# Kernel optimization log

Measured on AMD Instinct MI355X. Metric: run time of the kernel, lower is better.

Reference implementation:

```python
import jax, jax.numpy as jnp
import numpy as np
import math

N, D, H, E = 4096, 128, 8, 131072
HD = D // H  # head_dim = 16
SCALE = 1.0 / math.sqrt(HD)


def ln(x, g, b, eps=1e-5):
    m = x.mean(-1, keepdims=True)
    v = ((x - m) ** 2).mean(-1, keepdims=True)
    return (x - m) * jax.lax.rsqrt(v + eps) * g + b


def setup_inputs() -> dict:
    key = jax.random.key(0)
    ks = iter(jax.random.split(key, 40))

    def lin(out_d, in_d):
        w = jax.random.normal(next(ks), (out_d, in_d), jnp.float32) / math.sqrt(in_d)
        b = jnp.zeros((out_d,), jnp.float32)
        return w, b

    x = jax.random.normal(next(ks), (N, D), jnp.float32)
    edge_index = jax.random.randint(next(ks), (2, E), 0, N, dtype=jnp.int64)
    wq_l, bq_l = lin(D, D); wk_l, bk_l = lin(D, D); wv_l, bv_l = lin(D, D)
    wg, bg = lin(D, 2 * D)
    wq_g, bq_g = lin(D, D); wk_g, bk_g = lin(D, D); wv_g, bv_g = lin(D, D)
    wo_g, bo_g = lin(D, D)
    wf, bf = lin(D, 2 * D)
    gf = jnp.ones((D,), jnp.float32); betaf = jnp.zeros((D,), jnp.float32)
    w1, b1 = lin(4 * D, D); w2, b2 = lin(D, 4 * D)
    g1 = jnp.ones((D,), jnp.float32); be1 = jnp.zeros((D,), jnp.float32)
    g2 = jnp.ones((D,), jnp.float32); be2 = jnp.zeros((D,), jnp.float32)
    return dict(x=x, edge_index=edge_index,
                wq_l=wq_l, bq_l=bq_l, wk_l=wk_l, bk_l=bk_l, wv_l=wv_l, bv_l=bv_l,
                wg=wg, bg=bg,
                wq_g=wq_g, bq_g=bq_g, wk_g=wk_g, bk_g=bk_g, wv_g=wv_g, bv_g=bv_g,
                wo_g=wo_g, bo_g=bo_g,
                wf=wf, bf=bf, gf=gf, betaf=betaf,
                w1=w1, b1=b1, w2=w2, b2=b2,
                g1=g1, be1=be1, g2=g2, be2=be2)


def reference(x, edge_index, wq_l, bq_l, wk_l, bk_l, wv_l, bv_l, wg, bg,
              wq_g, bq_g, wk_g, bk_g, wv_g, bv_g, wo_g, bo_g,
              wf, bf, gf, betaf, w1, b1, w2, b2, g1, be1, g2, be2):
    src, dst = edge_index[0], edge_index[1]  # PyG: j=source, i=target
    # ---- local edge-indexed multi-head attention (GraphInteractionModule) ----
    Q = (x @ wq_l.T + bq_l).reshape(N, H, HD)
    K = (x @ wk_l.T + bk_l).reshape(N, H, HD)
    V = (x @ wv_l.T + bv_l).reshape(N, H, HD)
    attn = (Q[dst] * K[src]).sum(-1) * SCALE            # [E, H]
    m = jax.ops.segment_max(attn, dst, num_segments=N)  # [N, H]
    e = jnp.exp(attn - m[dst])
    s = jax.ops.segment_sum(e, dst, num_segments=N)
    alpha = e / s[dst]                                  # segment softmax over edges into each dst
    agg = jax.ops.segment_sum(V[src] * alpha[..., None], dst, num_segments=N).reshape(N, D)
    gate = jax.nn.sigmoid(jnp.concatenate([x, agg], axis=-1) @ wg.T + bg)
    local = gate * agg + (1.0 - gate) * x
    # ---- global dense MHA over all nodes (B=1) ----
    xn = ln(x, g1, be1)
    q = (xn @ wq_g.T + bq_g).reshape(N, H, HD)
    k = (xn @ wk_g.T + bk_g).reshape(N, H, HD)
    v = (xn @ wv_g.T + bv_g).reshape(N, H, HD)
    scores = jnp.einsum('nhd,mhd->hnm', q, k) * SCALE   # [H, N, N]
    p = jax.nn.softmax(scores, axis=-1)
    go = jnp.einsum('hnm,mhd->nhd', p, v).reshape(N, D) @ wo_g.T + bo_g
    # ---- fusion + residual + FFN ----
    fused = jax.nn.relu(ln(jnp.concatenate([local, go], axis=-1) @ wf.T + bf, gf, betaf))
    h = x + fused
    h2 = ln(h, g2, be2)
    out = h + (jax.nn.gelu(h2 @ w1.T + b1, approximate=False) @ w2.T + b2)
    return out
```

## Files before the change

kernel.cpp:

```cpp
#include <hip/hip_runtime.h>
#include <math.h>

#define NN 4096
#define DM 128
#define NE 131072
#define BCAP 96
#define QSCALE 0.36067376022224085f
#define ESCALE 0.36067376022224085f

typedef short short8 __attribute__((ext_vector_type(8)));
typedef float f32x4  __attribute__((ext_vector_type(4)));
typedef unsigned int uint4v __attribute__((ext_vector_type(4)));

static __device__ __forceinline__ unsigned pk2(float lo, float hi) {
  union { float f; unsigned u; } a, b; a.f = lo; b.f = hi;
  return __builtin_amdgcn_perm(b.u + 0x8000u, a.u + 0x8000u, 0x07060302u);
}
static __device__ __forceinline__ unsigned pkp(float lo, float hi) {
  union { float f; unsigned u; } a, b; a.f = lo; b.f = hi;
  return __builtin_amdgcn_perm(b.u, a.u, 0x07060302u);
}
static __device__ __forceinline__ unsigned short f2bh(float f) {
  union { float f; unsigned u; } v; v.f = f;
  return (unsigned short)((v.u + 0x8000u) >> 16);
}
static __device__ __forceinline__ float b2f16(unsigned short u) {
  union { unsigned u; float f; } v; v.u = ((unsigned)u) << 16; return v.f;
}
static __device__ __forceinline__ float blo(unsigned u) {
  union { unsigned u; float f; } v; v.u = u << 16; return v.f;
}
static __device__ __forceinline__ float bhi(unsigned u) {
  union { unsigned u; float f; } v; v.u = u & 0xffff0000u; return v.f;
}
static __device__ __forceinline__ short8 cvt8(float4 a, float4 b) {
  uint4v u;
  u.x = pk2(a.x, a.y); u.y = pk2(a.z, a.w);
  u.z = pk2(b.x, b.y); u.w = pk2(b.z, b.w);
  return __builtin_bit_cast(short8, u);
}
static __device__ __forceinline__ int detect64(const int* __restrict__ EI) {
  int v = EI[2 * (threadIdx.x & 63) + 1];
  for (int off = 1; off < 64; off <<= 1) v |= __shfl_xor(v, off);
  return (v == 0) ? 1 : 0;
}

__global__ __launch_bounds__(256) void k_fill(float* __restrict__ out, float v, int n) {
  int i = blockIdx.x * 256 + threadIdx.x;
  if (i < n) out[i] = v;
}

#define LN1(V, GV, BV) V = (V - mean) * rstd * GV + BV
__global__ __launch_bounds__(256) void gemm_six(
    const float* __restrict__ X,
    const float* __restrict__ G1, const float* __restrict__ Be1,
    const float* __restrict__ W0, const float* __restrict__ W1, const float* __restrict__ W2,
    const float* __restrict__ W3, const float* __restrict__ W4, const float* __restrict__ W5,
    const float* __restrict__ B0, const float* __restrict__ B1, const float* __restrict__ B2,
    const float* __restrict__ B3, const float* __restrict__ B4, const float* __restrict__ B5,
    void* __restrict__ O0, void* __restrict__ O1, void* __restrict__ O2,
    void* __restrict__ O3, void* __restrict__ O4, void* __restrict__ O5,
    int* __restrict__ deg,
    const float* __restrict__ WFp, const float* __restrict__ WOg, const float* __restrict__ BOg,
    float* __restrict__ WCp, float* __restrict__ BFp,
    const int* __restrict__ EI, int* __restrict__ EL)
{
  __shared__ short Asm[2][64][40];
  __shared__ short Wsm[2][64][40];
  if (blockIdx.y == 13) {
    int is64 = detect64(EI);
    int base = blockIdx.x * 2048 + threadIdx.x;
#pragma unroll
    for (int r = 0; r < 8; r++) {
      int e = base + r * 256;
      int d = is64 ? EI[2*(NE+e)] : EI[NE+e];
      d = min(max(d, 0), NN-1);
      int slot = atomicAdd(&deg[d], 1);
      if (slot < BCAP) EL[d * BCAP + slot] = e;
    }
    return;
  }
  if (blockIdx.y == 12) {
    if (blockIdx.x >= 16) return;
    const int c = threadIdx.x & 127;
    const int f0 = blockIdx.x * 8 + (threadIdx.x >> 7) * 4;
    const float* wf0 = WFp + (size_t)(f0 + 0) * 256 + 128;
    const float* wf1 = WFp + (size_t)(f0 + 1) * 256 + 128;
    const float* wf2 = WFp + (size_t)(f0 + 2) * 256 + 128;
    const float* wf3 = WFp + (size_t)(f0 + 3) * 256 + 128;
    float a0v = 0.f, a1v = 0.f, a2v = 0.f, a3v = 0.f;
    float c0 = 0.f, c1 = 0.f, c2 = 0.f, c3 = 0.f;
#pragma unroll 4
    for (int n = 0; n < 128; n++) {
      float wo = WOg[(size_t)n * 128 + c];
      float bv = BOg[n];
      float w0 = wf0[n], w1 = wf1[n], w2 = wf2[n], w3 = wf3[n];
      a0v += w0 * wo; a1v += w1 * wo; a2v += w2 * wo; a3v += w3 * wo;
      c0 += w0 * bv; c1 += w1 * bv; c2 += w2 * bv; c3 += w3 * bv;
    }
    WCp[(size_t)(f0 + 0) * 128 + c] = a0v;
    WCp[(size_t)(f0 + 1) * 128 + c] = a1v;
    WCp[(size_t)(f0 + 2) * 128 + c] = a2v;
    WCp[(size_t)(f0 + 3) * 128 + c] = a3v;
    if (c == 0) { BFp[f0] = c0; BFp[f0 + 1] = c1; BFp[f0 + 2] = c2; BFp[f0 + 3] = c3; }
    return;
  }
  const int g = blockIdx.y >> 1;
  const float* Wt  = (g==0)?W0:(g==1)?W1:(g==2)?W2:(g==3)?W3:(g==4)?W4:W5;
  const float* Bia = (g==0)?B0:(g==1)?B1:(g==2)?B2:(g==3)?B3:(g==4)?B4:B5;
  void* Cp         = (g==0)?O0:(g==1)?O1:(g==2)?O2:(g==3)?O3:(g==4)?O4:O5;
  const int omode  = (g==4)?3:(g==5)?2:1;
  const float osc  = (g==3)? QSCALE : (g==0)? ESCALE : 1.f;
  const int m0 = blockIdx.x * 64, n0 = (blockIdx.y & 1) * 64;
  const int tid = threadIdx.x;
  const int srow = tid >> 2, koff = (tid & 3) * 8;
  const int lane = tid & 63, wave = tid >> 6;
  const int quad = lane >> 4, m16 = lane & 15;

  const float* arow = X + (size_t)(m0 + srow) * 128 + koff;
  float4 a0[4], a1[4];
#pragma unroll
  for (int c = 0; c < 4; c++) {
    a0[c] = *(const float4*)(arow + c * 32);
    a1[c] = *(const float4*)(arow + c * 32 + 4);
  }
  if (g >= 3) {
    float s = 0.f;
#pragma unroll
    for (int c = 0; c < 4; c++)
      s += a0[c].x + a0[c].y + a0[c].z + a0[c].w + a1[c].x + a1[c].y + a1[c].z + a1[c].w;
    s += __shfl_xor(s, 1); s += __shfl_xor(s, 2);
    float mean = s * (1.0f / 128.0f);
    float v = 0.f;
#pragma unroll
    for (int c = 0; c < 4; c++) {
      float d;
      d = a0[c].x - mean; v += d*d;  d = a0[c].y - mean; v += d*d;
      d = a0[c].z - mean; v += d*d;  d = a0[c].w - mean; v += d*d;
      d = a1[c].x - mean; v += d*d;  d = a1[c].y - mean; v += d*d;
      d = a1[c].z - mean; v += d*d;  d = a1[c].w - mean; v += d*d;
    }
    v += __shfl_xor(v, 1); v += __shfl_xor(v, 2);
    float rstd = rsqrtf(v * (1.0f / 128.0f) + 1e-5f);
#pragma unroll
    for (int c = 0; c < 4; c++) {
      const int col = c * 32 + koff;
      float4 gv0 = *(const float4*)(G1 + col),  gv1 = *(const float4*)(G1 + col + 4);
      float4 bv0 = *(const float4*)(Be1 + col), bv1 = *(const float4*)(Be1 + col + 4);
      LN1(a0[c].x, gv0.x, bv0.x); LN1(a0[c].y, gv0.y, bv0.y);
      LN1(a0[c].z, gv0.z, bv0.z); LN1(a0[c].w, gv0.w, bv0.w);
      LN1(a1[c].x, gv1.x, bv1.x); LN1(a1[c].y, gv1.y, bv1.y);
      LN1(a1[c].z, gv1.z, bv1.z); LN1(a1[c].w, gv1.w, bv1.w);
    }
  }

  f32x4 acc[4];
#pragma unroll
  for (int i = 0; i < 4; i++) acc[i] = {0.f, 0.f, 0.f, 0.f};
  float4 w0r, w1r;
  {
    const float* wp = Wt + (size_t)(n0 + srow) * 128 + koff;
    w0r = *(const float4*)wp; w1r = *(const float4*)(wp + 4);
  }
#pragma unroll
  for (int c = 0; c < 4; c++) {
    const int cur = c & 1;
    *(short8*)&Asm[cur][srow][koff] = cvt8(a0[c], a1[c]);
    *(short8*)&Wsm[cur][srow][koff] = cvt8(w0r, w1r);
    __syncthreads();
    if (c < 3) {
      const float* wp = Wt + (size_t)(n0 + srow) * 128 + (c + 1) * 32 + koff;
      w0r = *(const float4*)wp; w1r = *(const float4*)(wp + 4);
    }
    short8 af = *(short8*)&Asm[cur][wave * 16 + m16][quad * 8];
#pragma unroll
    for (int nt = 0; nt < 4; nt++) {
      short8 bf = *(short8*)&Wsm[cur][nt * 16 + m16][quad * 8];
      acc[nt] = __builtin_amdgcn_mfma_f32_16x16x32_bf16(af, bf, acc[nt], 0, 0, 0);
    }
  }
#pragma unroll
  for (int nt = 0; nt < 4; nt++) {
#pragma unroll
    for (int r = 0; r < 4; r++) {
      const int m = m0 + wave * 16 + quad * 4 + r;
      const int n = n0 + nt * 16 + m16;
      float v = (acc[nt][r] + Bia[n]) * osc;
      size_t oi = (size_t)m * 128 + n;
      if (omode == 1)      ((unsigned short*)Cp)[oi] = f2bh(v);
      else if (omode == 3) ((unsigned short*)Cp)[(size_t)(n >> 4) * (NN * 16) + (size_t)m * 16 + (n & 15)] = f2bh(v);
      else                 ((unsigned short*)Cp)[(size_t)n * NN + m] = f2bh(v);
    }
  }
}

__global__ __launch_bounds__(512) void k_attn_agg(
    const unsigned short* __restrict__ Kh, const unsigned short* __restrict__ Qb,
    const unsigned short* __restrict__ VT, float* __restrict__ O,
    const int* __restrict__ EI, const int* __restrict__ deg, const int* __restrict__ elist,
    const unsigned short* __restrict__ Vl, const unsigned short* __restrict__ Kb,
    const unsigned short* __restrict__ Qb16, float* __restrict__ AG)
{
  __shared__ union {
    struct { float LO[8][4][16][16]; float LL[8][4][16]; } a;
    struct { float PS[4][128]; float SSH[4][2][8]; float SC[4][BCAP][8]; } g;
  } S;
  if (blockIdx.x >= 512) {
    int is64 = detect64(EI);
    int tid = threadIdx.x;
    int dsti = tid >> 7;
    int half = (tid >> 6) & 1;
    int lane = tid & 63;
    int d = (blockIdx.x - 512) * 4 + dsti;
    int degd = min(deg[d], BCAP), start = d * BCAP;
    int hh = lane >> 3;
    unsigned qv = *(const unsigned*)(Qb16 + (size_t)d * DM + 2 * lane);
    float q0 = blo(qv), q1 = bhi(qv);
    float ss = 0.f;
    int i = half;
    for (; i + 6 < degd; i += 8) {
      int e0 = elist[start+i], e1 = elist[start+i+2], e2 = elist[start+i+4], e3 = elist[start+i+6];
      e0 = min(max(e0,0),NE-1); e1 = min(max(e1,0),NE-1);
      e2 = min(max(e2,0),NE-1); e3 = min(max(e3,0),NE-1);
      int s0 = is64 ? EI[2*e0] : EI[e0];
      int s1 = is64 ? EI[2*e1] : EI[e1];
      int s2 = is64 ? EI[2*e2] : EI[e2];
      int s3 = is64 ? EI[2*e3] : EI[e3];
      s0 = min(max(s0,0),NN-1); s1 = min(max(s1,0),NN-1);
      s2 = min(max(s2,0),NN-1); s3 = min(max(s3,0),NN-1);
      unsigned k0 = *(const unsigned*)(Kb + (size_t)s0 * DM + 2 * lane);
      unsigned k1 = *(const unsigned*)(Kb + (size_t)s1 * DM + 2 * lane);
      unsigned k2 = *(const unsigned*)(Kb + (size_t)s2 * DM + 2 * lane);
      unsigned k3 = *(const unsigned*)(Kb + (size_t)s3 * DM + 2 * lane);
      float p0 = q0 * blo(k0) + q1 * bhi(k0);
      float p1 = q0 * blo(k1) + q1 * bhi(k1);
      float p2 = q0 * blo(k2) + q1 * bhi(k2);
      float p3 = q0 * blo(k3) + q1 * bhi(k3);
      p0 += __shfl_xor(p0,1); p0 += __shfl_xor(p0,2); p0 += __shfl_xor(p0,4);
      p1 += __shfl_xor(p1,1); p1 += __shfl_xor(p1,2); p1 += __shfl_xor(p1,4);
      p2 += __shfl_xor(p2,1); p2 += __shfl_xor(p2,2); p2 += __shfl_xor(p2,4);
      p3 += __shfl_xor(p3,1); p3 += __shfl_xor(p3,2); p3 += __shfl_xor(p3,4);
      float ev0 = __builtin_amdgcn_exp2f(fminf(p0, 43.0f));
      float ev1 = __builtin_amdgcn_exp2f(fminf(p1, 43.0f));
      float ev2 = __builtin_amdgcn_exp2f(fminf(p2, 43.0f));
      float ev3 = __builtin_amdgcn_exp2f(fminf(p3, 43.0f));
      if ((lane & 7) == 0) {
        S.g.SC[dsti][i][hh] = ev0;   S.g.SC[dsti][i+2][hh] = ev1;
        S.g.SC[dsti][i+4][hh] = ev2; S.g.SC[dsti][i+6][hh] = ev3;
      }
      ss += ev0 + ev1 + ev2 + ev3;
    }
    for (; i < degd; i += 2) {
      int e = elist[start + i];
      e = min(max(e,0),NE-1);
      int s = is64 ? EI[2*e] : EI[e];
      s = min(max(s, 0), NN-1);
      unsigned k = *(const unsigned*)(Kb + (size_t)s * DM + 2 * lane);
      float p = q0 * blo(k) + q1 * bhi(k);
      p += __shfl_xor(p,1); p += __shfl_xor(p,2); p += __shfl_xor(p,4);
      float ev = __builtin_amdgcn_exp2f(fminf(p, 43.0f));
      if ((lane & 7) == 0) S.g.SC[dsti][i][hh] = ev;
      ss += ev;
    }
    if ((lane & 7) == 0) S.g.SSH[dsti][half][hh] = ss;
    __syncthreads();
    float inv = 1.0f / fmaxf(S.g.SSH[dsti][0][hh] + S.g.SSH[dsti][1][hh], 1e-30f);
    float ax = 0.f, ay = 0.f;
    i = half;
    for (; i + 6 < degd; i += 8) {
      int e0 = elist[start+i], e1 = elist[start+i+2], e2 = elist[start+i+4], e3 = elist[start+i+6];
      e0 = min(max(e0,0),NE-1); e1 = min(max(e1,0),NE-1);
      e2 = min(max(e2,0),NE-1); e3 = min(max(e3,0),NE-1);
      int s0 = is64 ? EI[2*e0] : EI[e0];
      int s1 = is64 ? EI[2*e1] : EI[e1];
      int s2 = is64 ? EI[2*e2] : EI[e2];
      int s3 = is64 ? EI[2*e3] : EI[e3];
      s0 = min(max(s0,0),NN-1); s1 = min(max(s1,0),NN-1);
      s2 = min(max(s2,0),NN-1); s3 = min(max(s3,0),NN-1);
      float w0 = S.g.SC[dsti][i][hh] * inv;
      float w1 = S.g.SC[dsti][i+2][hh] * inv;
      float w2 = S.g.SC[dsti][i+4][hh] * inv;
      float w3 = S.g.SC[dsti][i+6][hh] * inv;
      unsigned v0 = *(const unsigned*)(Vl + (size_t)s0 * DM + 2 * lane);
      unsigned v1 = *(const unsigned*)(Vl + (size_t)s1 * DM + 2 * lane);
      unsigned v2 = *(const unsigned*)(Vl + (size_t)s2 * DM + 2 * lane);
      unsigned v3 = *(const unsigned*)(Vl + (size_t)s3 * DM + 2 * lane);
      ax += w0 * blo(v0) + w1 * blo(v1) + w2 * blo(v2) + w3 * blo(v3);
      ay += w0 * bhi(v0) + w1 * bhi(v1) + w2 * bhi(v2) + w3 * bhi(v3);
    }
    for (; i < degd; i += 2) {
      int e = elist[start + i];
      e = min(max(e,0),NE-1);
      int s = is64 ? EI[2*e] : EI[e];
      s = min(max(s, 0), NN-1);
      float a = S.g.SC[dsti][i][hh] * inv;
      unsigned v = *(const unsigned*)(Vl + (size_t)s * DM + 2 * lane);
      ax += a * blo(v);
      ay += a * bhi(v);
    }
    if (half == 1) { S.g.PS[dsti][2*lane] = ax; S.g.PS[dsti][2*lane+1] = ay; }
    __syncthreads();
    if (half == 0) {
      float2 r; r.x = ax + S.g.PS[dsti][2*lane]; r.y = ay + S.g.PS[dsti][2*lane+1];
      *(float2*)(AG + (size_t)d * DM + 2 * lane) = r;
    }
    return;
  }
  const int h = blockIdx.x >> 6, qt = blockIdx.x & 63;
  const int tid = threadIdx.x, lane = tid & 63, wave = tid >> 6;
  const int quad = lane >> 4, m16 = lane & 15;
  const int r0 = qt * 64;
  const short8 z8 = {0,0,0,0,0,0,0,0};
  const f32x4  z4 = {0.f,0.f,0.f,0.f};
  short8 qf[4] = {z8, z8, z8, z8};
  if (quad < 2) {
#pragma unroll
    for (int j = 0; j < 4; j++)
      qf[j] = *(const short8*)(Qb + (size_t)(r0 + j * 16 + m16) * DM + h * 16 + quad * 8);
  }
  short8 ones;
#pragma unroll
  for (int i = 0; i < 8; i++) ones[i] = (short)0x3F80;
  const int kperm = (m16 >> 2) * 8 + (m16 & 3);
  const int kbase = wave * 512;
  const unsigned short* khead = Kh + (size_t)h * (NN * 16);
  f32x4 acc[4] = {z4, z4, z4, z4};
  f32x4 acc2[4] = {z4, z4, z4, z4};
  short8 a0 = z8, a1 = z8, a2 = z8, a3 = z8;
  for (int kt = 0; kt < 8; kt++) {
    const int key0 = kbase + kt * 64;
    if (quad < 2) {
      const unsigned short* kp = khead + (size_t)(key0 + kperm) * 16 + quad * 8;
      a0 = *(const short8*)kp;
      a1 = *(const short8*)(kp + 4 * 16);
      a2 = *(const short8*)(kp + 32 * 16);
      a3 = *(const short8*)(kp + 36 * 16);
    }
    const unsigned short* vp = VT + (size_t)(h * 16 + m16) * NN + key0 + quad * 8;
    short8 av0 = *(const short8*)vp;
    short8 av1 = *(const short8*)(vp + 32);
#pragma unroll
    for (int j = 0; j < 4; j++) {
      f32x4 s0 = __builtin_amdgcn_mfma_f32_16x16x32_bf16(a0, qf[j], z4, 0, 0, 0);
      f32x4 s1 = __builtin_amdgcn_mfma_f32_16x16x32_bf16(a1, qf[j], z4, 0, 0, 0);
      f32x4 s2 = __builtin_amdgcn_mfma_f32_16x16x32_bf16(a2, qf[j], z4, 0, 0, 0);
      f32x4 s3 = __builtin_amdgcn_mfma_f32_16x16x32_bf16(a3, qf[j], z4, 0, 0, 0);
      float e0 = __builtin_amdgcn_exp2f(s0[0]), e1 = __builtin_amdgcn_exp2f(s0[1]);
      float e2 = __builtin_amdgcn_exp2f(s0[2]), e3 = __builtin_amdgcn_exp2f(s0[3]);
      float e4 = __builtin_amdgcn_exp2f(s1[0]), e5 = __builtin_amdgcn_exp2f(s1[1]);
      float e6 = __builtin_amdgcn_exp2f(s1[2]), e7 = __builtin_amdgcn_exp2f(s1[3]);
      uint4v u;
      u.x = pkp(e0, e1); u.y = pkp(e2, e3); u.z = pkp(e4, e5); u.w = pkp(e6, e7);
      short8 p0 = __builtin_bit_cast(short8, u);
      float f0 = __builtin_amdgcn_exp2f(s2[0]), f1 = __builtin_amdgcn_exp2f(s2[1]);
      float f2 = __builtin_amdgcn_exp2f(s2[2]), f3 = __builtin_amdgcn_exp2f(s2[3]);
      float f4 = __builtin_amdgcn_exp2f(s3[0]), f5 = __builtin_amdgcn_exp2f(s3[1]);
      float f6 = __builtin_amdgcn_exp2f(s3[2]), f7 = __builtin_amdgcn_exp2f(s3[3]);
      uint4v w;
      w.x = pkp(f0, f1); w.y = pkp(f2, f3); w.z = pkp(f4, f5); w.w = pkp(f6, f7);
      short8 p1 = __builtin_bit_cast(short8, w);
      acc[j]  = __builtin_amdgcn_mfma_f32_16x16x32_bf16(av0, p0, acc[j], 0, 0, 0);
      acc[j]  = __builtin_amdgcn_mfma_f32_16x16x32_bf16(av1, p1, acc[j], 0, 0, 0);
      acc2[j] = __builtin_amdgcn_mfma_f32_16x16x32_bf16(ones, p0, acc2[j], 0, 0, 0);
      acc2[j] = __builtin_amdgcn_mfma_f32_16x16x32_bf16(ones, p1, acc2[j], 0, 0, 0);
    }
  }
#pragma unroll
  for (int j = 0; j < 4; j++) {
    float4 a4; a4.x = acc[j][0]; a4.y = acc[j][1]; a4.z = acc[j][2]; a4.w = acc[j][3];
    *(float4*)&S.a.LO[wave][j][m16][quad * 4] = a4;
    if (lane < 16) S.a.LL[wave][j][lane] = acc2[j][0];
  }
  __syncthreads();
  if (wave < 4) {
    const int j = wave;
    float4 o = *(float4*)&S.a.LO[0][j][m16][quad * 4];
    float lt = S.a.LL[0][j][m16];
#pragma unroll
    for (int w2 = 1; w2 < 8; w2++) {
      float4 t = *(float4*)&S.a.LO[w2][j][m16][quad * 4];
      o.x += t.x; o.y += t.y; o.z += t.z; o.w += t.w;
      lt += S.a.LL[w2][j][m16];
    }
    float inv = 1.0f / fmaxf(lt, 1e-30f);
    float4 r4; r4.x = o.x * inv; r4.y = o.y * inv; r4.z = o.z * inv; r4.w = o.w * inv;
    *(float4*)(O + (size_t)(r0 + j * 16 + m16) * DM + h * 16 + quad * 4) = r4;
  }
}

__global__ __launch_bounds__(256) void gemm_gatefuse(
    const float* __restrict__ X, const float* __restrict__ AGG, const float* __restrict__ GO,
    const float* __restrict__ Wg, const float* __restrict__ Bg,
    const float* __restrict__ WF, const float* __restrict__ WC,
    const float* __restrict__ BF, const float* __restrict__ BFOLD,
    float* __restrict__ TMPF)
{
  __shared__ short Asm[64][40];
  __shared__ short Wsm[128][40];
  __shared__ short Lsm[4][64][40];
  const int m0 = blockIdx.x * 64, n0 = blockIdx.y * 64;
  const int tid = threadIdx.x;
  const int srow = tid >> 2, koff = (tid & 3) * 8;
  const int wrow = tid >> 1, koff2 = (tid & 1) * 16;
  const int lane = tid & 63, wave = tid >> 6;
  const int quad = lane >> 4, m16 = lane & 15;

  f32x4 acc8[8];
#pragma unroll
  for (int i = 0; i < 8; i++) acc8[i] = {0.f, 0.f, 0.f, 0.f};
  for (int k0 = 0; k0 < 256; k0 += 32) {
    const int kg = k0 + koff;
    const float* ap = (kg < 128) ? (X + (size_t)(m0 + srow) * 128 + kg)
                                 : (AGG + (size_t)(m0 + srow) * 128 + (kg - 128));
    float4 a0 = *(const float4*)ap, a1 = *(const float4*)(ap + 4);
    const float* wp = Wg + (size_t)wrow * 256 + k0 + koff2;
    float4 w0 = *(const float4*)wp,       float4w1 = *(const float4*)(wp + 4);
    float4 w2v = *(const float4*)(wp + 8), w3v = *(const float4*)(wp + 12);
    __syncthreads();
    *(short8*)&Asm[srow][koff] = cvt8(a0, a1);
    *(short8*)&Wsm[wrow][koff2]     = cvt8(w0, float4w1);
    *(short8*)&Wsm[wrow][koff2 + 8] = cvt8(w2v, w3v);
    __syncthreads();
    short8 af = *(short8*)&Asm[wave * 16 + m16][quad * 8];
#pragma unroll
    for (int nt = 0; nt < 8; nt++) {
      short8 bf = *(short8*)&Wsm[nt * 16 + m16][quad * 8];
      acc8[nt] = __builtin_amdgcn_mfma_f32_16x16x32_bf16(af, bf, acc8[nt], 0, 0, 0);
    }
  }
  __syncthreads();
#pragma unroll
  for (int nt = 0; nt < 8; nt++) {
#pragma unroll
    for (int r = 0; r < 4; r++) {
      const int mr = wave * 16 + quad * 4 + r;
      const int n = nt * 16 + m16;
      float v = acc8[nt][r] + Bg[n];
      size_t oi = (size_t)(m0 + mr) * 128 + n;
      float gg = 1.0f / (1.0f + __expf(fminf(fmaxf(-v, -80.f), 80.f)));
      float loc = gg * AGG[oi] + (1.0f - gg) * X[oi];
      Lsm[n >> 5][mr][n & 31] = (short)f2bh(loc);
    }
  }

  f32x4 acc[4];
#pragma unroll
  for (int i = 0; i < 4; i++) acc[i] = {0.f, 0.f, 0.f, 0.f};
  for (int k0 = 0; k0 < 256; k0 += 32) {
    const int c = k0 >> 5;
    float4 a0g, a1g;
    if (c >= 4) {
      const float* ap = GO + (size_t)(m0 + srow) * 128 + (k0 - 128) + koff;
      a0g = *(const float4*)ap; a1g = *(const float4*)(ap + 4);
    }
    const float* wp = (c < 4) ? (WF + (size_t)(n0 + srow) * 256 + k0 + koff)
                              : (WC + (size_t)(n0 + srow) * 128 + (k0 - 128) + koff);
    float4 w0 = *(const float4*)wp, w1v = *(const float4*)(wp + 4);
    __syncthreads();
    if (c >= 4) *(short8*)&Asm[srow][koff] = cvt8(a0g, a1g);
    *(short8*)&Wsm[srow][koff] = cvt8(w0, w1v);
    __syncthreads();
    short8 af = (c < 4) ? *(short8*)&Lsm[c][wave * 16 + m16][quad * 8]
                        : *(short8*)&Asm[wave * 16 + m16][quad * 8];
#pragma unroll
    for (int nt = 0; nt < 4; nt++) {
      short8 bf = *(short8*)&Wsm[nt * 16 + m16][quad * 8];
      acc[nt] = __builtin_amdgcn_mfma_f32_16x16x32_bf16(af, bf, acc[nt], 0, 0, 0);
    }
  }
#pragma unroll
  for (int nt = 0; nt < 4; nt++) {
#pragma unroll
    for (int r = 0; r < 4; r++) {
      const int m = m0 + wave * 16 + quad * 4 + r;
      const int n = n0 + nt * 16 + m16;
      TMPF[(size_t)m * 128 + n] = acc[nt][r] + BF[n] + BFOLD[n];
    }
  }
}

__global__ __launch_bounds__(256) void gemm_ffn1(
    const float* __restrict__ T, const float* __restrict__ X,
    const float* __restrict__ Gf, const float* __restrict__ Bef,
    const float* __restrict__ G2, const float* __restrict__ Be2,
    const float* __restrict__ W1, const float* __restrict__ B1,
    float* __restrict__ H, unsigned short* __restrict__ T1)
{
  __shared__ short Asm[2][64][40];
  __shared__ short Wsm[2][64][40];
  const int m0 = blockIdx.x * 64, n0 = blockIdx.y * 64;
  const int tid = threadIdx.x;
  const int srow = tid >> 2, koff = (tid & 3) * 8;
  const int lane = tid & 63, wave = tid >> 6;
  const int quad = lane >> 4, m16 = lane & 15;

  const float* trow = T + (size_t)(m0 + srow) * 128 + koff;
  const float* xrow = X + (size_t)(m0 + srow) * 128 + koff;
  float4 a0[4], a1[4];
#pragma unroll
  for (int c = 0; c < 4; c++) {
    a0[c] = *(const float4*)(trow + c * 32);
    a1[c] = *(const float4*)(trow + c * 32 + 4);
  }
  {
    float s = 0.f;
#pragma unroll
    for (int c = 0; c < 4; c++)
      s += a0[c].x + a0[c].y + a0[c].z + a0[c].w + a1[c].x + a1[c].y + a1[c].z + a1[c].w;
    s += __shfl_xor(s, 1); s += __shfl_xor(s, 2);
    float mean = s * (1.0f / 128.0f);
    float v = 0.f;
#pragma unroll
    for (int c = 0; c < 4; c++) {
      float d;
      d = a0[c].x - mean; v += d*d;  d = a0[c].y - mean; v += d*d;
      d = a0[c].z - mean; v += d*d;  d = a0[c].w - mean; v += d*d;
      d = a1[c].x - mean; v += d*d;  d = a1[c].y - mean; v += d*d;
      d = a1[c].z - mean; v += d*d;  d = a1[c].w - mean; v += d*d;
    }
    v += __shfl_xor(v, 1); v += __shfl_xor(v, 2);
    float rstd = rsqrtf(v * (1.0f / 128.0f) + 1e-5f);
#pragma unroll
    for (int c = 0; c < 4; c++) {
      const int col = c * 32 + koff;
      float4 gv0 = *(const float4*)(Gf + col),  gv1 = *(const float4*)(Gf + col + 4);
      float4 bv0 = *(const float4*)(Bef + col), bv1 = *(const float4*)(Bef + col + 4);
      float4 x0 = *(const float4*)(xrow + c * 32), x1 = *(const float4*)(xrow + c * 32 + 4);
      LN1(a0[c].x, gv0.x, bv0.x); LN1(a0[c].y, gv0.y, bv0.y);
      LN1(a0[c].z, gv0.z, bv0.z); LN1(a0[c].w, gv0.w, bv0.w);
      LN1(a1[c].x, gv1.x, bv1.x); LN1(a1[c].y, gv1.y, bv1.y);
      LN1(a1[c].z, gv1.z, bv1.z); LN1(a1[c].w, gv1.w, bv1.w);
      a0[c].x = x0.x + fmaxf(a0[c].x, 0.f); a0[c].y = x0.y + fmaxf(a0[c].y, 0.f);
      a0[c].z = x0.z + fmaxf(a0[c].z, 0.f); a0[c].w = x0.w + fmaxf(a0[c].w, 0.f);
      a1[c].x = x1.x + fmaxf(a1[c].x, 0.f); a1[c].y = x1.y + fmaxf(a1[c].y, 0.f);
      a1[c].z = x1.z + fmaxf(a1[c].z, 0.f); a1[c].w = x1.w + fmaxf(a1[c].w, 0.f);
      if (blockIdx.y == 0) {
        *(float4*)(H + (size_t)(m0 + srow) * 128 + c * 32 + koff)     = a0[c];
        *(float4*)(H + (size_t)(m0 + srow) * 128 + c * 32 + koff + 4) = a1[c];
      }
    }
  }
  {
    float s = 0.f;
#pragma unroll
    for (int c = 0; c < 4; c++)
      s += a0[c].x + a0[c].y + a0[c].z + a0[c].w + a1[c].x + a1[c].y + a1[c].z + a1[c].w;
    s += __shfl_xor(s, 1); s += __shfl_xor(s, 2);
    float mean = s * (1.0f / 128.0f);
    float v = 0.f;
#pragma unroll
    for (int c = 0; c < 4; c++) {
      float d;
      d = a0[c].x - mean; v += d*d;  d = a0[c].y - mean; v += d*d;
      d = a0[c].z - mean; v += d*d;  d = a0[c].w - mean; v += d*d;
      d = a1[c].x - mean; v += d*d;  d = a1[c].y - mean; v += d*d;
      d = a1[c].z - mean; v += d*d;  d = a1[c].w - mean; v += d*d;
    }
    v += __shfl_xor(v, 1); v += __shfl_xor(v, 2);
    float rstd = rsqrtf(v * (1.0f / 128.0f) + 1e-5f);
#pragma unroll
    for (int c = 0; c < 4; c++) {
      const int col = c * 32 + koff;
      float4 gv0 = *(const float4*)(G2 + col),  gv1 = *(const float4*)(G2 + col + 4);
      float4 bv0 = *(const float4*)(Be2 + col), bv1 = *(const float4*)(Be2 + col + 4);
      LN1(a0[c].x, gv0.x, bv0.x); LN1(a0[c].y, gv0.y, bv0.y);
      LN1(a0[c].z, gv0.z, bv0.z); LN1(a0[c].w, gv0.w, bv0.w);
      LN1(a1[c].x, gv1.x, bv1.x); LN1(a1[c].y, gv1.y, bv1.y);
      LN1(a1[c].z, gv1.z, bv1.z); LN1(a1[c].w, gv1.w, bv1.w);
    }
  }

  f32x4 acc[4];
#pragma unroll
  for (int i = 0; i < 4; i++) acc[i] = {0.f, 0.f, 0.f, 0.f};
  float4 w0r, w1r;
  {
    const float* wp = W1 + (size_t)(n0 + srow) * 128 + koff;
    w0r = *(const float4*)wp; w1r = *(const float4*)(wp + 4);
  }
#pragma unroll
  for (int c = 0; c < 4; c++) {
    const int cur = c & 1;
    *(short8*)&Asm[cur][srow][koff] = cvt8(a0[c], a1[c]);
    *(short8*)&Wsm[cur][srow][koff] = cvt8(w0r, w1r);
    __syncthreads();
    if (c < 3) {
      const float* wp = W1 + (size_t)(n0 + srow) * 128 + (c + 1) * 32 + koff;
      w0r = *(const float4*)wp; w1r = *(const float4*)(wp + 4);
    }
    short8 af = *(short8*)&Asm[cur][wave * 16 + m16][quad * 8];
#pragma unroll
    for (int nt = 0; nt < 4; nt++) {
      short8 bf = *(short8*)&Wsm[cur][nt * 16 + m16][quad * 8];
      acc[nt] = __builtin_amdgcn_mfma_f32_16x16x32_bf16(af, bf, acc[nt], 0, 0, 0);
    }
  }
#pragma unroll
  for (int nt = 0; nt < 4; nt++) {
#pragma unroll
    for (int r = 0; r < 4; r++) {
      const int m = m0 + wave * 16 + quad * 4 + r;
      const int n = n0 + nt * 16 + m16;
      float v = acc[nt][r] + B1[n];
      v = 0.5f * v * (1.0f + erff(v * 0.70710678118654752f));
      T1[(size_t)m * 512 + n] = f2bh(v);
    }
  }
}

__global__ __launch_bounds__(256) void gemm_w2b(
    const unsigned short* __restrict__ A,
    const float* __restrict__ Wt, const float* __restrict__ Bias,
    const float* __restrict__ Res, float* __restrict__ Cp)
{
  __shared__ short Asm[2][64][40];
  __shared__ short Wsm[2][64][40];
  const int m0 = blockIdx.x * 64, n0 = blockIdx.y * 64;
  const int tid = threadIdx.x;
  const int srow = tid >> 2, koff = (tid & 3) * 8;
  const int lane = tid & 63, wave = tid >> 6;
  const int quad = lane >> 4, m16 = lane & 15;
  f32x4 acc[4];
#pragma unroll
  for (int i = 0; i < 4; i++) acc[i] = {0.f, 0.f, 0.f, 0.f};

  short8 avr; float4 w0r, w1r;
  {
    avr = *(const short8*)(A + (size_t)(m0 + srow) * 512 + koff);
    const float* wp = Wt + (size_t)(n0 + srow) * 512 + koff;
    w0r = *(const float4*)wp; w1r = *(const float4*)(wp + 4);
  }
  for (int k0 = 0; k0 < 512; k0 += 32) {
    const int cur = (k0 >> 5) & 1;
    *(short8*)&Asm[cur][srow][koff] = avr;
    *(short8*)&Wsm[cur][srow][koff] = cvt8(w0r, w1r);
    __syncthreads();
    if (k0 + 32 < 512) {
      const int kg = k0 + 32 + koff;
      avr = *(const short8*)(A + (size_t)(m0 + srow) * 512 + kg);
      const float* wp = Wt + (size_t)(n0 + srow) * 512 + kg;
      w0r = *(const float4*)wp; w1r = *(const float4*)(wp + 4);
    }
    short8 af = *(short8*)&Asm[cur][wave * 16 + m16][quad * 8];
#pragma unroll
    for (int nt = 0; nt < 4; nt++) {
      short8 bf = *(short8*)&Wsm[cur][nt * 16 + m16][quad * 8];
      acc[nt] = __builtin_amdgcn_mfma_f32_16x16x32_bf16(af, bf, acc[nt], 0, 0, 0);
    }
  }
#pragma unroll
  for (int nt = 0; nt < 4; nt++) {
#pragma unroll
    for (int r = 0; r < 4; r++) {
      const int m = m0 + wave * 16 + quad * 4 + r;
      const int n = n0 + nt * 16 + m16;
      size_t oi = (size_t)m * 128 + n;
      Cp[oi] = acc[nt][r] + Bias[n] + Res[oi];
    }
  }
}

extern "C" void kernel_launch(void* const* d_in, const int* in_sizes, int n_in,
                              void* d_out, int out_size, void* d_ws, size_t ws_size,
                              hipStream_t stream) {
  const float* x     = (const float*)d_in[0];
  const int*   ei    = (const int*)  d_in[1];
  const float* wq_l  = (const float*)d_in[2];  const float* bq_l = (const float*)d_in[3];
  const float* wk_l  = (const float*)d_in[4];  const float* bk_l = (const float*)d_in[5];
  const float* wv_l  = (const float*)d_in[6];  const float* bv_l = (const float*)d_in[7];
  const float* wg    = (const float*)d_in[8];  const float* bg   = (const float*)d_in[9];
  const float* wq_g  = (const float*)d_in[10]; const float* bq_g = (const float*)d_in[11];
  const float* wk_g  = (const float*)d_in[12]; const float* bk_g = (const float*)d_in[13];
  const float* wv_g  = (const float*)d_in[14]; const float* bv_g = (const float*)d_in[15];
  const float* wo_g  = (const float*)d_in[16]; const float* bo_g = (const float*)d_in[17];
  const float* wf    = (const float*)d_in[18]; const float* bff  = (const float*)d_in[19];
  const float* gf    = (const float*)d_in[20]; const float* betaf= (const float*)d_in[21];
  const float* w1    = (const float*)d_in[22]; const float* b1   = (const float*)d_in[23];
  const float* w2    = (const float*)d_in[24]; const float* b2   = (const float*)d_in[25];
  const float* g1    = (const float*)d_in[26]; const float* be1  = (const float*)d_in[27];
  const float* g2    = (const float*)d_in[28]; const float* be2  = (const float*)d_in[29];
  float* out = (float*)d_out;

  const size_t NEED = (size_t)4223104 * 4;
  if (ws_size < NEED) {
    k_fill<<<2048, 256, 0, stream>>>(out, 100.0f, NN*DM);
    return;
  }

  float* W = (float*)d_ws;
  unsigned short* lQb   = (unsigned short*)(W + 0);
  unsigned short* lKb   = (unsigned short*)(W + 524288);
  unsigned short* lV    = (unsigned short*)(W + 1048576);
  float*          go    = W + 1835008;
  unsigned short* qgb   = (unsigned short*)(W + 2359296);
  unsigned short* kgb   = (unsigned short*)(W + 2621440);
  unsigned short* vgT   = (unsigned short*)(W + 2883584);
  float*          tmpf  = W + 1310720;
  float*          h     = W + 2621440;
  unsigned short* t1    = (unsigned short*)(W + 0);
  int* deg    = (int*)(W + 3145728);
  float* Wc    = W + 3289088;
  float* bfold = W + 3305472;
  int* elist96 = (int*)(W + 3305600);
  float*          agg   = W + 3698816;

  dim3 b256(256);

  hipMemsetAsync(deg, 0, NN * sizeof(int), stream);

  gemm_six<<<dim3(64,14), b256, 0, stream>>>(x, g1, be1,
      wq_l, wk_l, wv_l, wq_g, wk_g, wv_g,
      bq_l, bk_l, bv_l, bq_g, bk_g, bv_g,
      lQb, lKb, lV, qgb, kgb, vgT, deg,
      wf, wo_g, bo_g, Wc, bfold, ei, elist96);

  k_attn_agg<<<1536, dim3(512), 0, stream>>>(kgb, qgb, vgT, go, ei, deg, elist96,
                                             lV, lKb, lQb, agg);

  gemm_gatefuse<<<dim3(64,2), b256, 0, stream>>>(x, agg, go, wg, bg, wf, Wc, bff, bfold, tmpf);
  gemm_ffn1<<<dim3(64,8), b256, 0, stream>>>(tmpf, x, gf, betaf, g2, be2, w1, b1, h, t1);
  gemm_w2b<<<dim3(64,2), b256, 0, stream>>>(t1, w2, b2, h, out);
}
```

Baseline: 210.5 us.

## Prefetch next K/V tile in dense attention and cache edge sources in LDS

The dense attention loop now software-pipelines its global loads, fetching the next 64-key K and V fragments while the MFMAs run on the current ones, and raises wave priority around the MFMA block. The graph aggregation path stores each edge's resolved source index in shared memory during the score pass, so the value pass no longer re-reads elist and edge_index. The LO scratch array is padded to 20 columns to reduce LDS bank conflicts, and a variable name typo is fixed. The cost is more registers for the double-buffered fragments and more shared memory for the index cache, which could lower occupancy.

```diff
diff --git a/kernel.cpp b/kernel.cpp
--- a/kernel.cpp
+++ b/kernel.cpp
@@ -202,8 +202,8 @@
     const unsigned short* __restrict__ Qb16, float* __restrict__ AG)
 {
   __shared__ union {
-    struct { float LO[8][4][16][16]; float LL[8][4][16]; } a;
-    struct { float PS[4][128]; float SSH[4][2][8]; float SC[4][BCAP][8]; } g;
+    struct { float LO[8][4][16][20]; float LL[8][4][16]; } a;
+    struct { float PS[4][128]; float SSH[4][2][8]; float SC[4][BCAP][8]; int SI[4][BCAP]; } g;
   } S;
   if (blockIdx.x >= 512) {
     int is64 = detect64(EI);
@@ -228,6 +228,10 @@
       int s3 = is64 ? EI[2*e3] : EI[e3];
       s0 = min(max(s0,0),NN-1); s1 = min(max(s1,0),NN-1);
       s2 = min(max(s2,0),NN-1); s3 = min(max(s3,0),NN-1);
+      if (lane == 0) {
+        S.g.SI[dsti][i] = s0;   S.g.SI[dsti][i+2] = s1;
+        S.g.SI[dsti][i+4] = s2; S.g.SI[dsti][i+6] = s3;
+      }
       unsigned k0 = *(const unsigned*)(Kb + (size_t)s0 * DM + 2 * lane);
       unsigned k1 = *(const unsigned*)(Kb + (size_t)s1 * DM + 2 * lane);
       unsigned k2 = *(const unsigned*)(Kb + (size_t)s2 * DM + 2 * lane);
@@ -255,6 +259,7 @@
       e = min(max(e,0),NE-1);
       int s = is64 ? EI[2*e] : EI[e];
       s = min(max(s, 0), NN-1);
+      if (lane == 0) S.g.SI[dsti][i] = s;
       unsigned k = *(const unsigned*)(Kb + (size_t)s * DM + 2 * lane);
       float p = q0 * blo(k) + q1 * bhi(k);
       p += __shfl_xor(p,1); p += __shfl_xor(p,2); p += __shfl_xor(p,4);
@@ -268,15 +273,8 @@
     float ax = 0.f, ay = 0.f;
     i = half;
     for (; i + 6 < degd; i += 8) {
-      int e0 = elist[start+i], e1 = elist[start+i+2], e2 = elist[start+i+4], e3 = elist[start+i+6];
-      e0 = min(max(e0,0),NE-1); e1 = min(max(e1,0),NE-1);
-      e2 = min(max(e2,0),NE-1); e3 = min(max(e3,0),NE-1);
-      int s0 = is64 ? EI[2*e0] : EI[e0];
-      int s1 = is64 ? EI[2*e1] : EI[e1];
-      int s2 = is64 ? EI[2*e2] : EI[e2];
-      int s3 = is64 ? EI[2*e3] : EI[e3];
-      s0 = min(max(s0,0),NN-1); s1 = min(max(s1,0),NN-1);
-      s2 = min(max(s2,0),NN-1); s3 = min(max(s3,0),NN-1);
+      int s0 = S.g.SI[dsti][i],   s1 = S.g.SI[dsti][i+2];
+      int s2 = S.g.SI[dsti][i+4], s3 = S.g.SI[dsti][i+6];
       float w0 = S.g.SC[dsti][i][hh] * inv;
       float w1 = S.g.SC[dsti][i+2][hh] * inv;
       float w2 = S.g.SC[dsti][i+4][hh] * inv;
@@ -289,10 +287,7 @@
       ay += w0 * bhi(v0) + w1 * bhi(v1) + w2 * bhi(v2) + w3 * bhi(v3);
     }
     for (; i < degd; i += 2) {
-      int e = elist[start + i];
-      e = min(max(e,0),NE-1);
-      int s = is64 ? EI[2*e] : EI[e];
-      s = min(max(s, 0), NN-1);
+      int s = S.g.SI[dsti][i];
       float a = S.g.SC[dsti][i][hh] * inv;
       unsigned v = *(const unsigned*)(Vl + (size_t)s * DM + 2 * lane);
       ax += a * blo(v);
@@ -324,27 +319,44 @@
   const int kperm = (m16 >> 2) * 8 + (m16 & 3);
   const int kbase = wave * 512;
   const unsigned short* khead = Kh + (size_t)h * (NN * 16);
+  const unsigned short* vbase = VT + (size_t)(h * 16 + m16) * NN;
   f32x4 acc[4] = {z4, z4, z4, z4};
   f32x4 acc2[4] = {z4, z4, z4, z4};
-  short8 a0 = z8, a1 = z8, a2 = z8, a3 = z8;
+  short8 ca0 = z8, ca1 = z8, ca2 = z8, ca3 = z8, cv0, cv1;
+  {
+    if (quad < 2) {
+      const unsigned short* kp = khead + (size_t)(kbase + kperm) * 16 + quad * 8;
+      ca0 = *(const short8*)kp;
+      ca1 = *(const short8*)(kp + 4 * 16);
+      ca2 = *(const short8*)(kp + 32 * 16);
+      ca3 = *(const short8*)(kp + 36 * 16);
+    }
+    const unsigned short* vp = vbase + kbase + quad * 8;
+    cv0 = *(const short8*)vp;
+    cv1 = *(const short8*)(vp + 32);
+  }
   for (int kt = 0; kt < 8; kt++) {
-    const int key0 = kbase + kt * 64;
-    if (quad < 2) {
-      const unsigned short* kp = khead + (size_t)(key0 + kperm) * 16 + quad * 8;
-      a0 = *(const short8*)kp;
-      a1 = *(const short8*)(kp + 4 * 16);
-      a2 = *(const short8*)(kp + 32 * 16);
-      a3 = *(const short8*)(kp + 36 * 16);
-    }
-    const unsigned short* vp = VT + (size_t)(h * 16 + m16) * NN + key0 + quad * 8;
-    short8 av0 = *(const short8*)vp;
-    short8 av1 = *(const short8*)(vp + 32);
+    short8 na0 = z8, na1 = z8, na2 = z8, na3 = z8, nv0 = z8, nv1 = z8;
+    if (kt < 7) {
+      const int key1 = kbase + (kt + 1) * 64;
+      if (quad < 2) {
+        const unsigned short* kp = khead + (size_t)(key1 + kperm) * 16 + quad * 8;
+        na0 = *(const short8*)kp;
+        na1 = *(const short8*)(kp + 4 * 16);
+        na2 = *(const short8*)(kp + 32 * 16);
+        na3 = *(const short8*)(kp + 36 * 16);
+      }
+      const unsigned short* vp = vbase + key1 + quad * 8;
+      nv0 = *(const short8*)vp;
+      nv1 = *(const short8*)(vp + 32);
+    }
+    __builtin_amdgcn_s_setprio(1);
 #pragma unroll
     for (int j = 0; j < 4; j++) {
-      f32x4 s0 = __builtin_amdgcn_mfma_f32_16x16x32_bf16(a0, qf[j], z4, 0, 0, 0);
-      f32x4 s1 = __builtin_amdgcn_mfma_f32_16x16x32_bf16(a1, qf[j], z4, 0, 0, 0);
-      f32x4 s2 = __builtin_amdgcn_mfma_f32_16x16x32_bf16(a2, qf[j], z4, 0, 0, 0);
-      f32x4 s3 = __builtin_amdgcn_mfma_f32_16x16x32_bf16(a3, qf[j], z4, 0, 0, 0);
+      f32x4 s0 = __builtin_amdgcn_mfma_f32_16x16x32_bf16(ca0, qf[j], z4, 0, 0, 0);
+      f32x4 s1 = __builtin_amdgcn_mfma_f32_16x16x32_bf16(ca1, qf[j], z4, 0, 0, 0);
+      f32x4 s2 = __builtin_amdgcn_mfma_f32_16x16x32_bf16(ca2, qf[j], z4, 0, 0, 0);
+      f32x4 s3 = __builtin_amdgcn_mfma_f32_16x16x32_bf16(ca3, qf[j], z4, 0, 0, 0);
       float e0 = __builtin_amdgcn_exp2f(s0[0]), e1 = __builtin_amdgcn_exp2f(s0[1]);
       float e2 = __builtin_amdgcn_exp2f(s0[2]), e3 = __builtin_amdgcn_exp2f(s0[3]);
       float e4 = __builtin_amdgcn_exp2f(s1[0]), e5 = __builtin_amdgcn_exp2f(s1[1]);
@@ -359,11 +371,13 @@
       uint4v w;
       w.x = pkp(f0, f1); w.y = pkp(f2, f3); w.z = pkp(f4, f5); w.w = pkp(f6, f7);
       short8 p1 = __builtin_bit_cast(short8, w);
-      acc[j]  = __builtin_amdgcn_mfma_f32_16x16x32_bf16(av0, p0, acc[j], 0, 0, 0);
-      acc[j]  = __builtin_amdgcn_mfma_f32_16x16x32_bf16(av1, p1, acc[j], 0, 0, 0);
+      acc[j]  = __builtin_amdgcn_mfma_f32_16x16x32_bf16(cv0, p0, acc[j], 0, 0, 0);
+      acc[j]  = __builtin_amdgcn_mfma_f32_16x16x32_bf16(cv1, p1, acc[j], 0, 0, 0);
       acc2[j] = __builtin_amdgcn_mfma_f32_16x16x32_bf16(ones, p0, acc2[j], 0, 0, 0);
       acc2[j] = __builtin_amdgcn_mfma_f32_16x16x32_bf16(ones, p1, acc2[j], 0, 0, 0);
     }
+    __builtin_amdgcn_s_setprio(0);
+    ca0 = na0; ca1 = na1; ca2 = na2; ca3 = na3; cv0 = nv0; cv1 = nv1;
   }
 #pragma unroll
   for (int j = 0; j < 4; j++) {
@@ -414,11 +428,11 @@
                                  : (AGG + (size_t)(m0 + srow) * 128 + (kg - 128));
     float4 a0 = *(const float4*)ap, a1 = *(const float4*)(ap + 4);
     const float* wp = Wg + (size_t)wrow * 256 + k0 + koff2;
-    float4 w0 = *(const float4*)wp,       float4w1 = *(const float4*)(wp + 4);
+    float4 w0 = *(const float4*)wp,       w1v = *(const float4*)(wp + 4);
     float4 w2v = *(const float4*)(wp + 8), w3v = *(const float4*)(wp + 12);
     __syncthreads();
     *(short8*)&Asm[srow][koff] = cvt8(a0, a1);
-    *(short8*)&Wsm[wrow][koff2]     = cvt8(w0, float4w1);
+    *(short8*)&Wsm[wrow][koff2]     = cvt8(w0, w1v);
     *(short8*)&Wsm[wrow][koff2 + 8] = cvt8(w2v, w3v);
     __syncthreads();
     short8 af = *(short8*)&Asm[wave * 16 + m16][quad * 8];
```

Result: no change. 208.9 us (-0.8%).
